# Kernel optimization log

Measured on AMD Instinct MI355X. Metric: run time of the kernel, lower is better.

The kernel has to match this reference:

```python
import jax, jax.numpy as jnp
import numpy as np
from jax import lax

B, T, D, H, Z = 32, 64, 32, 256, 64  # batch, seq len (tau), n vars, hidden_dim, z_dim


def gru(x, h0, W_ih, b_ih, W_hh, b_hh):
    """PyTorch-convention GRU. x: [B,T,I], h0: [B,H], W_ih: [3H,I], W_hh: [3H,H].
    Returns (outputs [B,T,H], final hidden [B,H])."""
    gi = jnp.einsum('bti,gi->btg', x, W_ih) + b_ih  # precompute input gates [B,T,3H]

    def step(h, gi_t):
        gh = h @ W_hh.T + b_hh
        i_r, i_z, i_n = jnp.split(gi_t, 3, axis=-1)
        h_r, h_z, h_n = jnp.split(gh, 3, axis=-1)
        r = jax.nn.sigmoid(i_r + h_r)
        u = jax.nn.sigmoid(i_z + h_z)
        n = jnp.tanh(i_n + r * h_n)
        h_new = (1.0 - u) * n + u * h
        return h_new, h_new

    hT, outs = lax.scan(step, h0, jnp.swapaxes(gi, 0, 1))
    return jnp.swapaxes(outs, 0, 1), hT


def setup_inputs() -> dict:
    key = jax.random.key(0)
    ks = iter(jax.random.split(key, 32))
    r = lambda shape: jax.random.normal(next(ks), shape, jnp.float32) * 0.1
    inp = {
        'x_past': jax.random.normal(next(ks), (B, T, D), jnp.float32),
        'x_current': jax.random.normal(next(ks), (B, T, D), jnp.float32),
        'eps': jax.random.normal(next(ks), (B, Z), jnp.float32),
        # Encoder: GRU(D->H) + fc_mu, fc_logsigma (H->Z)
        'enc_Wih': r((3 * H, D)), 'enc_bih': r((3 * H,)),
        'enc_Whh': r((3 * H, H)), 'enc_bhh': r((3 * H,)),
        'enc_mu_w': r((Z, H)), 'enc_mu_b': r((Z,)),
        'enc_ls_w': r((Z, H)), 'enc_ls_b': r((Z,)),
        # re_fc: z -> h0
        'refc_w': r((H, Z)), 'refc_b': r((H,)),
        # Stacked per-head params (D heads)
        'Win': r((D, D, H)),               # W_in_list
        'h_Wih': r((D, 3 * H, H)), 'h_bih': r((D, 3 * H)),
        'h_Whh': r((D, 3 * H, H)), 'h_bhh': r((D, 3 * H)),
        'fc_w': r((D, 1, H)), 'fc_b': r((D, 1)),
    }
    return inp


def _forward(x_past, x_current, eps, enc_Wih, enc_bih, enc_Whh, enc_bhh,
             enc_mu_w, enc_mu_b, enc_ls_w, enc_ls_b, refc_w, refc_b,
             Win, h_Wih, h_bih, h_Whh, h_bhh, fc_w, fc_b):
    b = x_past.shape[0]
    # Encoder
    _, h = gru(x_past, jnp.zeros((b, H), x_past.dtype), enc_Wih, enc_bih, enc_Whh, enc_bhh)
    mu = h @ enc_mu_w.T + enc_mu_b
    logsig = h @ enc_ls_w.T + enc_ls_b
    z = mu + eps * jnp.exp(logsig)               # reparameterize (std = exp(logsig))
    h0 = jnp.tanh(z @ refc_w.T + refc_b)         # [B,H]
    # Teacher-forced decoder input
    dec_in = jnp.concatenate([x_past[:, -1:, :], x_current[:, :-1, :]], axis=1)  # [B,T,D]

    def head(Wp, Wih, bih, Whh, bhh, fw, fb):
        xt = jnp.einsum('btd,dh->bth', dec_in, Wp)   # causal input selection
        out, _ = gru(xt, h0, Wih, bih, Whh, bhh)
        return jnp.einsum('bth,oh->bto', out, fw) + fb  # [B,T,1]

    recon = jax.vmap(head)(Win, h_Wih, h_bih, h_Whh, h_bhh, fc_w, fc_b)  # [D,B,T,1]
    recon = jnp.transpose(recon[..., 0], (1, 2, 0))  # [B,T,D]
    return recon, mu, logsig


def reference(x_past, x_current, eps, enc_Wih, enc_bih, enc_Whh, enc_bhh,
              enc_mu_w, enc_mu_b, enc_ls_w, enc_ls_b, refc_w, refc_b,
              Win, h_Wih, h_bih, h_Whh, h_bhh, fc_w, fc_b):
    return _forward(x_past, x_current, eps, enc_Wih, enc_bih, enc_Whh, enc_bhh,
                    enc_mu_w, enc_mu_b, enc_ls_w, enc_ls_b, refc_w, refc_b,
                    Win, h_Wih, h_bih, h_Whh, h_bhh, fc_w, fc_b)
```

## Files before the change

### kernel.cpp

```cpp
#include <hip/hip_runtime.h>
#include <math.h>

constexpr int NB = 32, NT = 64, ND = 32, NH = 256, NZ = 64, NG = 768;

constexpr long long OFF_HENC  = 0;
constexpr long long OFF_H0    = OFF_HENC + NB * NH;
constexpr long long OFF_BCMB  = OFF_H0 + NB * NH;
constexpr long long OFF_BIN   = OFF_BCMB + ND * 2 * NH;
constexpr long long OFF_BHN   = OFF_BIN + ND * NH;
constexpr long long OFF_EBC   = OFF_BHN + ND * NH;
constexpr long long OFF_WHH2  = OFF_EBC + 1024;
constexpr long long OFF_WC2   = OFF_WHH2 + (long long)32 * 768 * 256 / 2;
constexpr long long OFF_EWHH2 = OFF_WC2 + (long long)32 * 768 * 32 / 2;
constexpr long long OFF_EWI3  = OFF_EWHH2 + 768 * 256 / 2;
constexpr long long OFF_DINIMG= OFF_EWI3 + 768 * 32 / 2;
constexpr long long OFF_EXIMG = OFF_DINIMG + 64 * 1024 / 2;
constexpr long long WS_FLOATS = OFF_EXIMG + 64 * 1024 / 2;

typedef __attribute__((ext_vector_type(8))) short bf16x8;
typedef __attribute__((ext_vector_type(4))) float f32x4;

__device__ __forceinline__ float sigm(float x) { return 1.f / (1.f + __expf(-x)); }
__device__ __forceinline__ ushort f2b(float x) {
  unsigned u = __float_as_uint(x);
  unsigned r = (u + 0x7FFFu + ((u >> 16) & 1u)) >> 16;
  return (ushort)r;
}

__global__ void k_pre(const float* __restrict__ hWhh, const float* __restrict__ hbih,
                      const float* __restrict__ hbhh, const float* __restrict__ eWhh,
                      const float* __restrict__ eWih, const float* __restrict__ ebih,
                      const float* __restrict__ ebhh, float* __restrict__ ws) {
  int stride = gridDim.x * blockDim.x;
  int idx = blockIdx.x * blockDim.x + threadIdx.x;
  unsigned* img = (unsigned*)(ws + OFF_WHH2);
  for (int i = idx; i < 32 * 768 * 128; i += stride) {
    int e0 = 2 * i;
    img[i] = (unsigned)f2b(hWhh[e0]) | ((unsigned)f2b(hWhh[e0 + 1]) << 16);
  }
  for (int i = idx; i < ND * NH; i += stride) {
    int d = i >> 8, j = i & 255;
    const float* bi = hbih + d * NG;
    const float* bh = hbhh + d * NG;
    ws[OFF_BCMB + d * 512 + j]       = bi[j] + bh[j];
    ws[OFF_BCMB + d * 512 + 256 + j] = bi[256 + j] + bh[256 + j];
    ws[OFF_BIN + i] = bi[512 + j];
    ws[OFF_BHN + i] = bh[512 + j];
  }
  unsigned* eimg = (unsigned*)(ws + OFF_EWHH2);
  for (int i = idx; i < 768 * 128; i += stride) {
    int e0 = 2 * i;
    eimg[i] = (unsigned)f2b(eWhh[e0]) | ((unsigned)f2b(eWhh[e0 + 1]) << 16);
  }
  unsigned* eimg2 = (unsigned*)(ws + OFF_EWI3);
  for (int i = idx; i < 768 * 16; i += stride) {
    int byte = 4 * i;
    int g = byte >> 6;
    int nominal = byte ^ ((g & 3) << 4);
    int dd0 = (nominal & 63) >> 1;
    eimg2[i] = (unsigned)f2b(eWih[g * 32 + dd0]) | ((unsigned)f2b(eWih[g * 32 + dd0 + 1]) << 16);
  }
  for (int i = idx; i < 256; i += stride) {
    ws[OFF_EBC + i]       = ebih[i] + ebhh[i];
    ws[OFF_EBC + 256 + i] = ebih[256 + i] + ebhh[256 + i];
    ws[OFF_EBC + 512 + i] = ebih[512 + i];
    ws[OFF_EBC + 768 + i] = ebhh[512 + i];
  }
}

__global__ __launch_bounds__(256)
void k_wcomb(const float* __restrict__ Win, const float* __restrict__ hWih,
             float* __restrict__ ws) {
  __shared__ float wd_s[32 * 257];
  __shared__ float wih_s[32 * 257];
  int blk = blockIdx.x;
  int d = blk / 24, gsec = blk - d * 24;
  int tid = threadIdx.x;
  for (int i = tid; i < 32 * 256; i += 256) {
    int r = i >> 8, h = i & 255;
    wd_s[r * 257 + h]  = Win[((long long)(d * 32 + r)) * 256 + h];
    wih_s[r * 257 + h] = hWih[((long long)(d * NG + gsec * 32 + r)) * 256 + h];
  }
  __syncthreads();
  ushort* wcimg = (ushort*)(ws + OFF_WC2);
  for (int o = tid; o < 1024; o += 256) {
    int gl = o >> 5, dd = o & 31;
    float acc = 0.f;
    #pragma unroll 4
    for (int h = 0; h < 256; ++h) acc += wih_s[gl * 257 + h] * wd_s[dd * 257 + h];
    int g = gsec * 32 + gl;
    int off = (g * 64 + dd * 2) ^ ((g & 3) << 4);
    wcimg[d * 24576 + (off >> 1)] = f2b(acc);
  }
}

__global__ void k_misc(const float* __restrict__ xp, const float* __restrict__ xc,
                       float* __restrict__ ws) {
  int idx = blockIdx.x * blockDim.x + threadIdx.x;
  int i2 = idx & 32767;
  int t = i2 >> 9, lw = i2 & 511;
  int byte = lw * 4;
  int b = byte >> 6;
  int nominal = byte ^ ((b & 3) << 4);
  int dd0 = (nominal & 63) >> 1;
  if (idx < 32768) {
    float v0, v1;
    if (t == 0) { v0 = xp[(b * NT + 63) * ND + dd0]; v1 = xp[(b * NT + 63) * ND + dd0 + 1]; }
    else { v0 = xc[(b * NT + (t - 1)) * ND + dd0]; v1 = xc[(b * NT + (t - 1)) * ND + dd0 + 1]; }
    ((unsigned*)(ws + OFF_DINIMG))[i2] = (unsigned)f2b(v0) | ((unsigned)f2b(v1) << 16);
  } else {
    float v0 = xp[(b * NT + t) * ND + dd0];
    float v1 = xp[(b * NT + t) * ND + dd0 + 1];
    ((unsigned*)(ws + OFF_EXIMG))[i2] = (unsigned)f2b(v0) | ((unsigned)f2b(v1) << 16);
  }
}


__global__ __launch_bounds__(512, 1)
void k_enc6(float* __restrict__ ws) {
  __shared__ __align__(16) char l_wc[49152];
  __shared__ __align__(16) char l_hbf[4096];
  __shared__ __align__(16) char l_x[512];
  __shared__ float rz_s[512 * 9];
  __shared__ float in_s[256 * 9];
  __shared__ float ahn_s[256 * 9];
  __shared__ float hm[8 * 260];
  __shared__ float bias_s[1024];

  const int bg = blockIdx.x;
  const int tid = threadIdx.x, lane = tid & 63, w = tid >> 6;

  {
    const uint4* sc = (const uint4*)((const ushort*)(ws + OFF_EWI3));
    for (int i = tid; i < 3072; i += 512) ((uint4*)l_wc)[i] = sc[i];
    for (int i = tid; i < 1024; i += 512) bias_s[i] = ws[OFF_EBC + i];
  }
  for (int o = tid; o < 2048; o += 512) {
    int b = o >> 8, j = o & 255;
    hm[b * 260 + j] = 0.f;
    int bo = (b * 512 + j * 2) ^ ((b & 7) << 4);
    *(ushort*)(l_hbf + bo) = 0;
  }

  const ushort* wimg = (const ushort*)(ws + OFF_EWHH2);
  bf16x8 wf[6][8];
  {
    const int kob = (lane >> 4) * 8;
    #pragma unroll
    for (int u = 0; u < 6; ++u) {
      int rt = 16 * (u >> 1) + 2 * w + (u & 1);
      int row = rt * 16 + (lane & 15);
      #pragma unroll
      for (int kc = 0; kc < 8; ++kc)
        wf[u][kc] = *(const bf16x8*)(wimg + row * 256 + kc * 32 + kob);
    }
  }
  __syncthreads();

  const int colL = lane & 15;
  const int rowB = lane & 7;
  const int kb16 = (lane >> 4) * 16;

  for (int t = 0; t < 64; ++t) {
    if (tid >= 480) {
      int c = tid - 480;
      ((uint4*)l_x)[c] = ((const uint4*)((const char*)(ws + OFF_EXIMG) + t * 2048 + bg * 512))[c];
    }
    __syncthreads();

    f32x4 acc[6];
    #pragma unroll
    for (int u = 0; u < 6; ++u) acc[u] = (f32x4){0.f, 0.f, 0.f, 0.f};
    #pragma unroll
    for (int kc = 0; kc < 8; ++kc) {
      bf16x8 bf = *(const bf16x8*)(l_hbf + ((rowB * 512 + kc * 64 + kb16) ^ (rowB << 4)));
      #pragma unroll
      for (int u = 0; u < 6; ++u)
        acc[u] = __builtin_amdgcn_mfma_f32_16x16x32_bf16(wf[u][kc], bf, acc[u], 0, 0, 0);
    }
    bf16x8 bx = *(const bf16x8*)(l_x + ((rowB * 64 + kb16) ^ ((rowB & 3) << 4)));
    #pragma unroll
    for (int u = 0; u < 6; ++u) {
      int rt = 16 * (u >> 1) + 2 * w + (u & 1);
      int gA = rt * 16 + colL;
      f32x4 zero = {0.f, 0.f, 0.f, 0.f};
      bf16x8 aw = *(const bf16x8*)(l_wc + ((gA * 64 + kb16) ^ ((gA & 3) << 4)));
      f32x4 ai = __builtin_amdgcn_mfma_f32_16x16x32_bf16(aw, bx, zero, 0, 0, 0);
      if (colL < 8) {
        int r0 = rt * 16 + (lane >> 4) * 4;
        #pragma unroll
        for (int rg = 0; rg < 4; ++rg) {
          int g = r0 + rg;
          if (u < 4) rz_s[g * 9 + colL] = acc[u][rg] + ai[rg];
          else { in_s[(g - 512) * 9 + colL] = ai[rg]; ahn_s[(g - 512) * 9 + colL] = acc[u][rg]; }
        }
      }
    }
    __syncthreads();

    #pragma unroll
    for (int it = 0; it < 4; ++it) {
      int o = it * 512 + tid;
      int b = o >> 8, j = o & 255;
      float pr = rz_s[j * 9 + b] + bias_s[j];
      float pz = rz_s[(256 + j) * 9 + b] + bias_s[256 + j];
      float pni = in_s[j * 9 + b] + bias_s[512 + j];
      float pnh = ahn_s[j * 9 + b] + bias_s[768 + j];
      float r = sigm(pr), u = sigm(pz);
      float n = tanhf(pni + r * pnh);
      float hold = hm[b * 260 + j];
      float hv = (1.f - u) * n + u * hold;
      hm[b * 260 + j] = hv;
      int bo = (b * 512 + j * 2) ^ ((b & 7) << 4);
      *(ushort*)(l_hbf + bo) = f2b(hv);
    }
    __syncthreads();
  }
  for (int o = tid; o < 2048; o += 512) {
    int b = o >> 8, j = o & 255;
    ws[OFF_HENC + (bg * 8 + b) * 256 + j] = hm[b * 260 + j];
  }
}

__global__ __launch_bounds__(256)
void k_latent(const float* __restrict__ muw, const float* __restrict__ mub,
              const float* __restrict__ lsw, const float* __restrict__ lsb,
              const float* __restrict__ refw, const float* __restrict__ refb,
              const float* __restrict__ eps, float* __restrict__ ws,
              float* __restrict__ out) {
  __shared__ float hs[NH];
  __shared__ float mu_s[NZ];
  __shared__ float ls_s[NZ];
  __shared__ float zs[NZ];
  int b = blockIdx.x, tid = threadIdx.x;
  hs[tid] = ws[OFF_HENC + b * NH + tid];
  __syncthreads();
  if (tid < 128) {
    int zi = tid & 63;
    const float* w = (tid < 64 ? muw : lsw) + zi * NH;
    float acc = 0.f;
    #pragma unroll 4
    for (int k = 0; k < NH; ++k) acc += w[k] * hs[k];
    if (tid < 64) {
      acc += mub[zi];
      out[NB * NT * ND + b * NZ + zi] = acc;
      mu_s[zi] = acc;
    } else {
      acc += lsb[zi];
      out[NB * NT * ND + NB * NZ + b * NZ + zi] = acc;
      ls_s[zi] = acc;
    }
  }
  __syncthreads();
  if (tid < 64) zs[tid] = mu_s[tid] + eps[b * NZ + tid] * __expf(ls_s[tid]);
  __syncthreads();
  {
    const float* w = refw + tid * NZ;
    float acc = 0.f;
    #pragma unroll 4
    for (int q = 0; q < 64; ++q) acc += w[q] * zs[q];
    ws[OFF_H0 + b * NH + tid] = tanhf(acc + refb[tid]);
  }
}

__global__ __launch_bounds__(512, 1)
void k_dec6(const float* __restrict__ fcw, const float* __restrict__ fcb,
            float* __restrict__ ws, float* __restrict__ out) {
  __shared__ __align__(16) char l_wc[49152];
  __shared__ __align__(16) char l_hbf[4096];
  __shared__ __align__(16) char l_din[512];
  __shared__ float rz_s[512 * 9];
  __shared__ float in_s[256 * 9];
  __shared__ float ahn_s[256 * 9];
  __shared__ float hm[8 * 260];
  __shared__ float bias_s[1280];

  const int d = blockIdx.x & 31, bg = blockIdx.x >> 5;
  const int tid = threadIdx.x, lane = tid & 63, w = tid >> 6;

  {
    const uint4* sc = (const uint4*)((const ushort*)(ws + OFF_WC2) + d * 24576);
    for (int i = tid; i < 3072; i += 512) ((uint4*)l_wc)[i] = sc[i];
    for (int i = tid; i < 1280; i += 512)
      bias_s[i] = (i < 512)  ? ws[OFF_BCMB + d * 512 + i]
                : (i < 768)  ? ws[OFF_BIN + d * 256 + (i - 512)]
                : (i < 1024) ? ws[OFF_BHN + d * 256 + (i - 768)]
                             : fcw[d * 256 + (i - 1024)];
  }
  for (int o = tid; o < 2048; o += 512) {
    int b = o >> 8, j = o & 255;
    float v = ws[OFF_H0 + (bg * 8 + b) * 256 + j];
    hm[b * 260 + j] = v;
    int bo = (b * 512 + j * 2) ^ ((b & 7) << 4);
    *(ushort*)(l_hbf + bo) = f2b(v);
  }

  const ushort* wimg = (const ushort*)(ws + OFF_WHH2) + (long long)d * 196608;
  bf16x8 wf[6][8];
  {
    const int kob = (lane >> 4) * 8;
    #pragma unroll
    for (int u = 0; u < 6; ++u) {
      int rt = 16 * (u >> 1) + 2 * w + (u & 1);
      int row = rt * 16 + (lane & 15);
      #pragma unroll
      for (int kc = 0; kc < 8; ++kc)
        wf[u][kc] = *(const bf16x8*)(wimg + row * 256 + kc * 32 + kob);
    }
  }
  const float fcbd = fcb[d];
  __syncthreads();

  const int colL = lane & 15;
  const int rowB = lane & 7;
  const int kb16 = (lane >> 4) * 16;

  for (int t = 0; t < 64; ++t) {
    if (tid >= 480) {
      int c = tid - 480;
      ((uint4*)l_din)[c] = ((const uint4*)((const char*)(ws + OFF_DINIMG) + t * 2048 + bg * 512))[c];
    }
    __syncthreads();

    f32x4 acc[6];
    #pragma unroll
    for (int u = 0; u < 6; ++u) acc[u] = (f32x4){0.f, 0.f, 0.f, 0.f};
    #pragma unroll
    for (int kc = 0; kc < 8; ++kc) {
      bf16x8 bf = *(const bf16x8*)(l_hbf + ((rowB * 512 + kc * 64 + kb16) ^ (rowB << 4)));
      #pragma unroll
      for (int u = 0; u < 6; ++u)
        acc[u] = __builtin_amdgcn_mfma_f32_16x16x32_bf16(wf[u][kc], bf, acc[u], 0, 0, 0);
    }
    bf16x8 bx = *(const bf16x8*)(l_din + ((rowB * 64 + kb16) ^ ((rowB & 3) << 4)));
    #pragma unroll
    for (int u = 0; u < 6; ++u) {
      int rt = 16 * (u >> 1) + 2 * w + (u & 1);
      int gA = rt * 16 + colL;
      f32x4 zero = {0.f, 0.f, 0.f, 0.f};
      bf16x8 aw = *(const bf16x8*)(l_wc + ((gA * 64 + kb16) ^ ((gA & 3) << 4)));
      f32x4 ai = __builtin_amdgcn_mfma_f32_16x16x32_bf16(aw, bx, zero, 0, 0, 0);
      if (colL < 8) {
        int r0 = rt * 16 + (lane >> 4) * 4;
        #pragma unroll
        for (int rg = 0; rg < 4; ++rg) {
          int g = r0 + rg;
          if (u < 4) rz_s[g * 9 + colL] = acc[u][rg] + ai[rg];
          else { in_s[(g - 512) * 9 + colL] = ai[rg]; ahn_s[(g - 512) * 9 + colL] = acc[u][rg]; }
        }
      }
    }
    __syncthreads();

    #pragma unroll
    for (int it = 0; it < 4; ++it) {
      int o = it * 512 + tid;
      int b = o >> 8, j = o & 255;
      float pr = rz_s[j * 9 + b] + bias_s[j];
      float pz = rz_s[(256 + j) * 9 + b] + bias_s[256 + j];
      float pni = in_s[j * 9 + b] + bias_s[512 + j];
      float pnh = ahn_s[j * 9 + b] + bias_s[768 + j];
      float r = sigm(pr), u = sigm(pz);
      float n = tanhf(pni + r * pnh);
      float hold = hm[b * 260 + j];
      float hv = (1.f - u) * n + u * hold;
      hm[b * 260 + j] = hv;
      int bo = (b * 512 + j * 2) ^ ((b & 7) << 4);
      *(ushort*)(l_hbf + bo) = f2b(hv);
    }
    __syncthreads();

    if (tid < 64) {
      int b = tid >> 3, c = tid & 7;
      float p = 0.f;
      #pragma unroll
      for (int q = 0; q < 32; ++q) {
        int j = c * 32 + q;
        p += hm[b * 260 + j] * bias_s[1024 + j];
      }
      p += __shfl_down(p, 4);
      p += __shfl_down(p, 2);
      p += __shfl_down(p, 1);
      if (c == 0) out[((bg * 8 + b) * NT + t) * ND + d] = p + fcbd;
    }
  }
}

extern "C" void kernel_launch(void* const* d_in, const int* in_sizes, int n_in,
                              void* d_out, int out_size, void* d_ws, size_t ws_size,
                              hipStream_t stream) {
  const float* x_past = (const float*)d_in[0];
  const float* x_curr = (const float*)d_in[1];
  const float* eps    = (const float*)d_in[2];
  const float* eWih   = (const float*)d_in[3];
  const float* ebih   = (const float*)d_in[4];
  const float* eWhh   = (const float*)d_in[5];
  const float* ebhh   = (const float*)d_in[6];
  const float* muw    = (const float*)d_in[7];
  const float* mub    = (const float*)d_in[8];
  const float* lsw    = (const float*)d_in[9];
  const float* lsb    = (const float*)d_in[10];
  const float* refw   = (const float*)d_in[11];
  const float* refb   = (const float*)d_in[12];
  const float* Win    = (const float*)d_in[13];
  const float* hWih   = (const float*)d_in[14];
  const float* hbih   = (const float*)d_in[15];
  const float* hWhh   = (const float*)d_in[16];
  const float* hbhh   = (const float*)d_in[17];
  const float* fcw    = (const float*)d_in[18];
  const float* fcb    = (const float*)d_in[19];
  float* ws  = (float*)d_ws;
  float* out = (float*)d_out;

  if (ws_size < (size_t)WS_FLOATS * 4) return;

  k_pre   <<<2048, 256, 0, stream>>>(hWhh, hbih, hbhh, eWhh, eWih, ebih, ebhh, ws);
  k_wcomb <<<768, 256, 0, stream>>>(Win, hWih, ws);
  k_misc  <<<256, 256, 0, stream>>>(x_past, x_curr, ws);
  k_enc6  <<<4, 512, 0, stream>>>(ws);
  k_latent<<<NB, 256, 0, stream>>>(muw, mub, lsw, lsb, refw, refb, eps, ws, out);
  k_dec6  <<<128, 512, 0, stream>>>(fcw, fcb, ws, out);
}
```

Before: 853.1 us.

## Preload all timestep inputs into LDS, use fast tanh, parallelize FC reduction

Both the encoder and decoder recurrent kernels now load the whole 64-step input image into shared memory once, before the time loop. This removes one global load and one block barrier from every step. tanhf is replaced by an exp-based approximation, and the per-step output dot product is spread across all 8 waves with a full-wave shuffle reduction instead of using one wave. Launch bounds change to allow 2 blocks per CU, and the hm row stride changes to 264. The cost is about 32KB more LDS per block and slightly different tanh accuracy.

```diff
diff --git a/kernel.cpp b/kernel.cpp
--- a/kernel.cpp
+++ b/kernel.cpp
@@ -21,6 +21,11 @@
 typedef __attribute__((ext_vector_type(4))) float f32x4;
 
 __device__ __forceinline__ float sigm(float x) { return 1.f / (1.f + __expf(-x)); }
+__device__ __forceinline__ float tanhfast(float y) {
+  float e = __expf(-2.f * fabsf(y));
+  float th = 1.f - 2.f * e / (1.f + e);
+  return __builtin_copysignf(th, y);
+}
 __device__ __forceinline__ ushort f2b(float x) {
   unsigned u = __float_as_uint(x);
   unsigned r = (u + 0x7FFFu + ((u >> 16) & 1u)) >> 16;
@@ -116,15 +121,15 @@
 }
 
 
-__global__ __launch_bounds__(512, 1)
-void k_enc6(float* __restrict__ ws) {
+__global__ __launch_bounds__(512, 2)
+void k_enc7(float* __restrict__ ws) {
   __shared__ __align__(16) char l_wc[49152];
   __shared__ __align__(16) char l_hbf[4096];
-  __shared__ __align__(16) char l_x[512];
+  __shared__ __align__(16) char l_x[32768];
   __shared__ float rz_s[512 * 9];
   __shared__ float in_s[256 * 9];
   __shared__ float ahn_s[256 * 9];
-  __shared__ float hm[8 * 260];
+  __shared__ float hm[8 * 264];
   __shared__ float bias_s[1024];
 
   const int bg = blockIdx.x;
@@ -134,10 +139,15 @@
     const uint4* sc = (const uint4*)((const ushort*)(ws + OFF_EWI3));
     for (int i = tid; i < 3072; i += 512) ((uint4*)l_wc)[i] = sc[i];
     for (int i = tid; i < 1024; i += 512) bias_s[i] = ws[OFF_EBC + i];
+    const uint4* sx = (const uint4*)((const ushort*)(ws + OFF_EXIMG));
+    for (int i = tid; i < 2048; i += 512) {
+      int t = i >> 5, c = i & 31;
+      ((uint4*)l_x)[i] = sx[t * 128 + bg * 32 + c];
+    }
   }
   for (int o = tid; o < 2048; o += 512) {
     int b = o >> 8, j = o & 255;
-    hm[b * 260 + j] = 0.f;
+    hm[b * 264 + j] = 0.f;
     int bo = (b * 512 + j * 2) ^ ((b & 7) << 4);
     *(ushort*)(l_hbf + bo) = 0;
   }
@@ -162,12 +172,6 @@
   const int kb16 = (lane >> 4) * 16;
 
   for (int t = 0; t < 64; ++t) {
-    if (tid >= 480) {
-      int c = tid - 480;
-      ((uint4*)l_x)[c] = ((const uint4*)((const char*)(ws + OFF_EXIMG) + t * 2048 + bg * 512))[c];
-    }
-    __syncthreads();
-
     f32x4 acc[6];
     #pragma unroll
     for (int u = 0; u < 6; ++u) acc[u] = (f32x4){0.f, 0.f, 0.f, 0.f};
@@ -178,7 +182,7 @@
       for (int u = 0; u < 6; ++u)
         acc[u] = __builtin_amdgcn_mfma_f32_16x16x32_bf16(wf[u][kc], bf, acc[u], 0, 0, 0);
     }
-    bf16x8 bx = *(const bf16x8*)(l_x + ((rowB * 64 + kb16) ^ ((rowB & 3) << 4)));
+    bf16x8 bx = *(const bf16x8*)(l_x + t * 512 + ((rowB * 64 + kb16) ^ ((rowB & 3) << 4)));
     #pragma unroll
     for (int u = 0; u < 6; ++u) {
       int rt = 16 * (u >> 1) + 2 * w + (u & 1);
@@ -207,10 +211,10 @@
       float pni = in_s[j * 9 + b] + bias_s[512 + j];
       float pnh = ahn_s[j * 9 + b] + bias_s[768 + j];
       float r = sigm(pr), u = sigm(pz);
-      float n = tanhf(pni + r * pnh);
-      float hold = hm[b * 260 + j];
+      float n = tanhfast(pni + r * pnh);
+      float hold = hm[b * 264 + j];
       float hv = (1.f - u) * n + u * hold;
-      hm[b * 260 + j] = hv;
+      hm[b * 264 + j] = hv;
       int bo = (b * 512 + j * 2) ^ ((b & 7) << 4);
       *(ushort*)(l_hbf + bo) = f2b(hv);
     }
@@ -218,7 +222,7 @@
   }
   for (int o = tid; o < 2048; o += 512) {
     int b = o >> 8, j = o & 255;
-    ws[OFF_HENC + (bg * 8 + b) * 256 + j] = hm[b * 260 + j];
+    ws[OFF_HENC + (bg * 8 + b) * 256 + j] = hm[b * 264 + j];
   }
 }
 
@@ -263,16 +267,16 @@
   }
 }
 
-__global__ __launch_bounds__(512, 1)
-void k_dec6(const float* __restrict__ fcw, const float* __restrict__ fcb,
+__global__ __launch_bounds__(512, 2)
+void k_dec7(const float* __restrict__ fcw, const float* __restrict__ fcb,
             float* __restrict__ ws, float* __restrict__ out) {
   __shared__ __align__(16) char l_wc[49152];
   __shared__ __align__(16) char l_hbf[4096];
-  __shared__ __align__(16) char l_din[512];
+  __shared__ __align__(16) char l_din[32768];
   __shared__ float rz_s[512 * 9];
   __shared__ float in_s[256 * 9];
   __shared__ float ahn_s[256 * 9];
-  __shared__ float hm[8 * 260];
+  __shared__ float hm[8 * 264];
   __shared__ float bias_s[1280];
 
   const int d = blockIdx.x & 31, bg = blockIdx.x >> 5;
@@ -286,11 +290,16 @@
                 : (i < 768)  ? ws[OFF_BIN + d * 256 + (i - 512)]
                 : (i < 1024) ? ws[OFF_BHN + d * 256 + (i - 768)]
                              : fcw[d * 256 + (i - 1024)];
+    const uint4* sx = (const uint4*)((const ushort*)(ws + OFF_DINIMG));
+    for (int i = tid; i < 2048; i += 512) {
+      int t = i >> 5, c = i & 31;
+      ((uint4*)l_din)[i] = sx[t * 128 + bg * 32 + c];
+    }
   }
   for (int o = tid; o < 2048; o += 512) {
     int b = o >> 8, j = o & 255;
     float v = ws[OFF_H0 + (bg * 8 + b) * 256 + j];
-    hm[b * 260 + j] = v;
+    hm[b * 264 + j] = v;
     int bo = (b * 512 + j * 2) ^ ((b & 7) << 4);
     *(ushort*)(l_hbf + bo) = f2b(v);
   }
@@ -316,12 +325,6 @@
   const int kb16 = (lane >> 4) * 16;
 
   for (int t = 0; t < 64; ++t) {
-    if (tid >= 480) {
-      int c = tid - 480;
-      ((uint4*)l_din)[c] = ((const uint4*)((const char*)(ws + OFF_DINIMG) + t * 2048 + bg * 512))[c];
-    }
-    __syncthreads();
-
     f32x4 acc[6];
     #pragma unroll
     for (int u = 0; u < 6; ++u) acc[u] = (f32x4){0.f, 0.f, 0.f, 0.f};
@@ -332,7 +335,7 @@
       for (int u = 0; u < 6; ++u)
         acc[u] = __builtin_amdgcn_mfma_f32_16x16x32_bf16(wf[u][kc], bf, acc[u], 0, 0, 0);
     }
-    bf16x8 bx = *(const bf16x8*)(l_din + ((rowB * 64 + kb16) ^ ((rowB & 3) << 4)));
+    bf16x8 bx = *(const bf16x8*)(l_din + t * 512 + ((rowB * 64 + kb16) ^ ((rowB & 3) << 4)));
     #pragma unroll
     for (int u = 0; u < 6; ++u) {
       int rt = 16 * (u >> 1) + 2 * w + (u & 1);
@@ -361,27 +364,26 @@
       float pni = in_s[j * 9 + b] + bias_s[512 + j];
       float pnh = ahn_s[j * 9 + b] + bias_s[768 + j];
       float r = sigm(pr), u = sigm(pz);
-      float n = tanhf(pni + r * pnh);
-      float hold = hm[b * 260 + j];
+      float n = tanhfast(pni + r * pnh);
+      float hold = hm[b * 264 + j];
       float hv = (1.f - u) * n + u * hold;
-      hm[b * 260 + j] = hv;
+      hm[b * 264 + j] = hv;
       int bo = (b * 512 + j * 2) ^ ((b & 7) << 4);
       *(ushort*)(l_hbf + bo) = f2b(hv);
     }
     __syncthreads();
 
-    if (tid < 64) {
-      int b = tid >> 3, c = tid & 7;
-      float p = 0.f;
-      #pragma unroll
-      for (int q = 0; q < 32; ++q) {
-        int j = c * 32 + q;
-        p += hm[b * 260 + j] * bias_s[1024 + j];
-      }
+    {
+      float4 hv4 = *(const float4*)(hm + w * 264 + 4 * lane);
+      float4 fw4 = *(const float4*)(bias_s + 1024 + 4 * lane);
+      float p = hv4.x * fw4.x + hv4.y * fw4.y + hv4.z * fw4.z + hv4.w * fw4.w;
+      p += __shfl_down(p, 32);
+      p += __shfl_down(p, 16);
+      p += __shfl_down(p, 8);
       p += __shfl_down(p, 4);
       p += __shfl_down(p, 2);
       p += __shfl_down(p, 1);
-      if (c == 0) out[((bg * 8 + b) * NT + t) * ND + d] = p + fcbd;
+      if (lane == 0) out[((bg * 8 + w) * NT + t) * ND + d] = p + fcbd;
     }
   }
 }
@@ -417,7 +419,7 @@
   k_pre   <<<2048, 256, 0, stream>>>(hWhh, hbih, hbhh, eWhh, eWih, ebih, ebhh, ws);
   k_wcomb <<<768, 256, 0, stream>>>(Win, hWih, ws);
   k_misc  <<<256, 256, 0, stream>>>(x_past, x_curr, ws);
-  k_enc6  <<<4, 512, 0, stream>>>(ws);
+  k_enc7  <<<4, 512, 0, stream>>>(ws);
   k_latent<<<NB, 256, 0, stream>>>(muw, mub, lsw, lsb, refw, refb, eps, ws, out);
-  k_dec6  <<<128, 512, 0, stream>>>(fcw, fcb, ws, out);
-}
+  k_dec7  <<<128, 512, 0, stream>>>(fcw, fcb, ws, out);
+}
```

Measured after the change: 810.1 us. -5.0%, faster.
